# Performance work log

Hardware: AMD Instinct MI355X
Metric: run time of the kernel (lower is better)

The kernel has to match this reference:

```python
import jax, jax.numpy as jnp
import numpy as np

# dims: batch, samples, agents, obs_dim, action_dim, hidden
B, S, N, D, A, H = 512, 64, 8, 64, 16, 256
IN_DIM = (D + A) * N  # 640


def mish(x):
    return x * jnp.tanh(jax.nn.softplus(x))


def setup_inputs() -> dict:
    key = jax.random.key(0)
    ks = jax.random.split(key, 9)
    u = lambda k, shape, fan_in: jax.random.uniform(
        k, shape, jnp.float32, -1.0 / np.sqrt(fan_in), 1.0 / np.sqrt(fan_in))
    return {
        "state": jax.random.normal(ks[0], (B, N, D), jnp.float32),
        "action": jax.random.normal(ks[1], (B, N, A), jnp.float32),
        "W1": u(ks[2], (IN_DIM, H), IN_DIM),
        "b1": u(ks[3], (H,), IN_DIM),
        "W2": u(ks[4], (H, H), H),
        "b2": u(ks[5], (H,), H),
        "W3": u(ks[6], (H, 1), H),
        "b3": u(ks[7], (1,), H),
        # random grand-coalition permutations of the N agents, per (batch, sample)
        "perm": jnp.argsort(jax.random.uniform(ks[8], (B, S, N)), axis=-1).astype(jnp.int32),
    }


def reference(state, action, W1, b1, W2, b2, W3, b3, perm):
    # subcoalition mask [B,S,N,N]: torch builds one-hot(perm) @ tril(ones),
    # i.e. mask[b,s,i,j] = 1 iff j <= perm[b,s,i]
    subcoal = (jnp.arange(N) <= perm[..., None]).astype(state.dtype)
    # gathered actions in coalition order [B,S,N,A]: act_g[b,s,j] = action[b, perm[b,s,j]]
    act_g = action[jnp.arange(B)[:, None, None], perm]
    # masked subcoalition actions [B,S,N,N,A] -> [B,S,N,N*A]
    act = (act_g[:, :, None, :, :] * subcoal[..., None]).reshape(B, S, N, N * A)
    # flattened global obs broadcast over (sample, agent) axes [B,S,N,N*D]
    obs = jnp.broadcast_to(state.reshape(B, 1, 1, N * D), (B, S, N, N * D))
    x = jnp.concatenate([obs, act], axis=-1)  # [B,S,N,IN_DIM]
    # per-agent loop in torch uses shared q1 weights -> single batched MLP
    h = mish(x @ W1 + b1)
    h = mish(h @ W2 + b2)
    q = h @ W3 + b3                   # [B,S,N,1]
    q1 = q.mean(axis=1).squeeze(-1)   # mean over samples -> [B,N]
    return (q1, q1)
```

## Files before the change

### kernel.cpp

```cpp
#include <hip/hip_runtime.h>

typedef unsigned short ushort_t;
typedef _Float16 half_t;
typedef __attribute__((ext_vector_type(2))) _Float16 half2_t;
typedef __attribute__((ext_vector_type(8))) _Float16 half8_t;
typedef __attribute__((ext_vector_type(2))) __fp16 fp16x2;
typedef __attribute__((ext_vector_type(2))) float fx2;
typedef __attribute__((ext_vector_type(4))) float floatx4;

#define LOG2E 1.4426950408889634f
#define LN2   0.6931471805599453f

__device__ __forceinline__ float exp2_(float x) {
#if __has_builtin(__builtin_amdgcn_exp2f)
    return __builtin_amdgcn_exp2f(x);
#else
    return exp2f(x);
#endif
}

__device__ __forceinline__ half2_t cvt_pk_f16(float a, float b) {
    auto r = __builtin_amdgcn_cvt_pkrtz(a, b);
    return __builtin_bit_cast(half2_t, r);
}

__device__ __forceinline__ float fdot2_(half2_t a, half2_t b) {
#if __has_builtin(__builtin_amdgcn_fdot2)
    return __builtin_amdgcn_fdot2(__builtin_bit_cast(fp16x2, a),
                                  __builtin_bit_cast(fp16x2, b), 0.0f, false);
#else
    return (float)a.x * (float)b.x + (float)a.y * (float)b.y;
#endif
}

__device__ __forceinline__ fx2 mish2(fx2 t0) {
    fx2 one = {1.0f, 1.0f};
    fx2 m2  = {-2.0f, -2.0f};
    fx2 u   = {exp2_(t0.x), exp2_(t0.y)};
    fx2 s   = u + one;
    fx2 wv  = __builtin_elementwise_fma(s, s, one);
    fx2 rr  = {__builtin_amdgcn_rcpf(wv.x), __builtin_amdgcn_rcpf(wv.y)};
    fx2 v   = __builtin_elementwise_fma(rr, m2, one);
    return t0 * v;
}

__device__ __forceinline__ float dpp_sum16(float v) {
    int x = __float_as_int(v);
    v += __int_as_float(__builtin_amdgcn_update_dpp(0, x, 0xB1, 0xF, 0xF, true));
    x = __float_as_int(v);
    v += __int_as_float(__builtin_amdgcn_update_dpp(0, x, 0x4E, 0xF, 0xF, true));
    x = __float_as_int(v);
    v += __int_as_float(__builtin_amdgcn_update_dpp(0, x, 0x124, 0xF, 0xF, true));
    x = __float_as_int(v);
    v += __int_as_float(__builtin_amdgcn_update_dpp(0, x, 0x128, 0xF, 0xF, true));
    return v;
}

__global__ __launch_bounds__(256) void prep_kernel(
        const float* __restrict__ state,
        const float* __restrict__ action,
        const float* __restrict__ W1,
        const float* __restrict__ b1,
        const float* __restrict__ W2,
        float* __restrict__ obsW,
        half_t* __restrict__ actW,
        half_t* __restrict__ W2T,
        float* __restrict__ out) {
    int bid = blockIdx.x;
    int t = threadIdx.x;
    if (bid < 512) {
        int b = bid;
        const float* stp = state + (size_t)b * 512;
        const float* w1p = W1 + t;
        float a0 = 0.f, a1 = 0.f, a2 = 0.f, a3 = 0.f;
#pragma unroll 8
        for (int f = 0; f < 512; f += 4) {
            a0 = fmaf(stp[f + 0], w1p[(f + 0) * 256], a0);
            a1 = fmaf(stp[f + 1], w1p[(f + 1) * 256], a1);
            a2 = fmaf(stp[f + 2], w1p[(f + 2) * 256], a2);
            a3 = fmaf(stp[f + 3], w1p[(f + 3) * 256], a3);
        }
        obsW[b * 256 + t] = ((a0 + a1) + (a2 + a3) + b1[t]) * LOG2E;
    } else if (bid < 2560) {
        int idx = bid - 512;
        int j = idx & 7;
        int b0 = (idx >> 3) * 2;
        const float* W1a = W1 + (size_t)(512 + j * 16) * 256;
        float wv[16];
#pragma unroll
        for (int a = 0; a < 16; ++a) wv[a] = W1a[a * 256 + t];
#pragma unroll
        for (int bb = 0; bb < 2; ++bb) {
            int b = b0 + bb;
            const float* acp = action + (size_t)b * 128;
            float acc[8];
#pragma unroll
            for (int n = 0; n < 8; ++n) acc[n] = 0.f;
#pragma unroll
            for (int a = 0; a < 16; ++a) {
#pragma unroll
                for (int n = 0; n < 8; ++n)
                    acc[n] = fmaf(acp[n * 16 + a], wv[a], acc[n]);
            }
#pragma unroll
            for (int n = 0; n < 8; ++n)
                actW[(((size_t)b * 8 + n) * 8 + j) * 256 + t] = (half_t)(acc[n] * LOG2E);
        }
    } else {
        int blk = bid - 2560;
        if (blk < 16) {
            out[blk * 512 + t] = 0.0f;
            out[blk * 512 + 256 + t] = 0.0f;
        }
        int n = blk * 8 + (t >> 5);
        int klo = t & 31;
#pragma unroll
        for (int kk = 0; kk < 8; ++kk) {
            int k = kk * 32 + klo;
            W2T[n * 256 + k] = (half_t)W2[k * 256 + n];
        }
    }
}

#define CHUNK_US 528

__global__ __launch_bounds__(512, 4) void main_kernel(
        const float* __restrict__ obsW, const half_t* __restrict__ actW,
        const half_t* __restrict__ W2T, const int* __restrict__ perm,
        const float* __restrict__ b2,
        const float* __restrict__ W3, const float* __restrict__ b3,
        float* __restrict__ out) {
    __shared__ __align__(16) ushort_t h1[2][32 * CHUNK_US];
    __shared__ __align__(16) float obsb[256];
    __shared__ int perm_s[128];
    __shared__ float qpart[2][8][64];

    int t = threadIdx.x;
    int bid = blockIdx.x;
    int b = (bid & 7) * 64 + ((bid >> 3) & 63);
    int sgp = bid >> 9;
    int s0 = sgp * 16;

    int w = t >> 6;
    int L = t & 63;
    int lo = L & 15;
    int q = L >> 4;

    if (t < 256) obsb[t] = obsW[b * 256 + t];
    else if (t < 384) perm_s[t - 256] = perm[((size_t)b * 64 + s0) * 8 + (t - 256)];

    const half_t* w2base = W2T + ((size_t)(w * 32 + lo)) * 256 + q * 8;
    half8_t bpre[4];
    bpre[0] = *reinterpret_cast<const half8_t*>(w2base + 0 * 4096 + 0 * 32);
    bpre[1] = *reinterpret_cast<const half8_t*>(w2base + 1 * 4096 + 0 * 32);
    bpre[2] = *reinterpret_cast<const half8_t*>(w2base + 0 * 4096 + 1 * 32);
    bpre[3] = *reinterpret_cast<const half8_t*>(w2base + 1 * 4096 + 1 * 32);

    int g = L >> 1;
    int ksg = g >> 2;
    int qq = g & 3;
    int halfsel = L & 1;
    const half_t* actg = actW + (size_t)b * 64 * 256 + L * 4;
    int dstoff = qq * 128 + halfsel * 4 + ksg * CHUNK_US;

    __syncthreads();

    float4 ob = *reinterpret_cast<const float4*>(obsb + L * 4);

    {
        uint2 av[8];
#pragma unroll
        for (int j = 0; j < 8; ++j) {
            int p = perm_s[(0 * 8 + w) * 8 + j];
            av[j] = *reinterpret_cast<const uint2*>(actg + (p * 8 + j) * 256);
        }
        fx2 r01 = {ob.x, ob.y};
        fx2 r23 = {ob.z, ob.w};
        ushort_t* dst0 = h1[0] + dstoff;
#pragma unroll
        for (int j = 0; j < 8; ++j) {
            half2_t a0 = __builtin_bit_cast(half2_t, av[j].x);
            half2_t a1 = __builtin_bit_cast(half2_t, av[j].y);
            r01 += (fx2){(float)a0.x, (float)a0.y};
            r23 += (fx2){(float)a1.x, (float)a1.y};
            fx2 h01 = mish2(r01);
            fx2 h23 = mish2(r23);
            int row = w * 8 + j;
            int mt2 = row >> 4, lr = row & 15;
            uint2 pk = make_uint2(__builtin_bit_cast(unsigned, cvt_pk_f16(h01.x, h01.y)),
                                  __builtin_bit_cast(unsigned, cvt_pk_f16(h23.x, h23.y)));
            *reinterpret_cast<uint2*>(dst0 + mt2 * 8 * CHUNK_US + lr * 8) = pk;
        }
    }
    __syncthreads();

    floatx4 acc0[4][2];
#pragma unroll
    for (int mt = 0; mt < 4; ++mt)
#pragma unroll
        for (int nt = 0; nt < 2; ++nt) acc0[mt][nt] = (floatx4){0.f, 0.f, 0.f, 0.f};
    {
        uint2 av[8];
#pragma unroll
        for (int j = 0; j < 8; ++j) {
            int p = perm_s[(1 * 8 + w) * 8 + j];
            av[j] = *reinterpret_cast<const uint2*>(actg + (p * 8 + j) * 256);
        }
        fx2 r01 = {ob.x, ob.y};
        fx2 r23 = {ob.z, ob.w};
        ushort_t* dst1 = h1[1] + dstoff;
        const ushort_t* h1b0 = h1[0] + L * 8;
#pragma unroll
        for (int ks = 0; ks < 8; ++ks) {
            half8_t afr[4];
#pragma unroll
            for (int mt = 0; mt < 4; ++mt)
                afr[mt] = *reinterpret_cast<const half8_t*>(h1b0 + (mt * 8 + ks) * CHUNK_US);
            half8_t bfr0 = (ks == 0) ? bpre[0] : (ks == 1) ? bpre[2]
                         : *reinterpret_cast<const half8_t*>(w2base + 0 * 4096 + ks * 32);
            half8_t bfr1 = (ks == 0) ? bpre[1] : (ks == 1) ? bpre[3]
                         : *reinterpret_cast<const half8_t*>(w2base + 1 * 4096 + ks * 32);
#pragma unroll
            for (int mt = 0; mt < 4; ++mt) {
                acc0[mt][0] = __builtin_amdgcn_mfma_f32_16x16x32_f16(afr[mt], bfr0, acc0[mt][0], 0, 0, 0);
                acc0[mt][1] = __builtin_amdgcn_mfma_f32_16x16x32_f16(afr[mt], bfr1, acc0[mt][1], 0, 0, 0);
            }
            {
                half2_t a0 = __builtin_bit_cast(half2_t, av[ks].x);
                half2_t a1 = __builtin_bit_cast(half2_t, av[ks].y);
                r01 += (fx2){(float)a0.x, (float)a0.y};
                r23 += (fx2){(float)a1.x, (float)a1.y};
                fx2 h01 = mish2(r01);
                fx2 h23 = mish2(r23);
                int row = w * 8 + ks;
                int mt2 = row >> 4, lr = row & 15;
                uint2 pk = make_uint2(__builtin_bit_cast(unsigned, cvt_pk_f16(h01.x, h01.y)),
                                      __builtin_bit_cast(unsigned, cvt_pk_f16(h23.x, h23.y)));
                *reinterpret_cast<uint2*>(dst1 + mt2 * 8 * CHUNK_US + lr * 8) = pk;
            }
        }
    }
    __syncthreads();

    int col0 = w * 32 + 0 * 16 + lo;
    int col1 = w * 32 + 1 * 16 + lo;
    fx2 b2p = {b2[col0] * LOG2E, b2[col1] * LOG2E};
    half2_t w3p = cvt_pk_f16(W3[col0] * LN2, W3[col1] * LN2);

    floatx4 acc1[4][2];
#pragma unroll
    for (int mt = 0; mt < 4; ++mt)
#pragma unroll
        for (int nt = 0; nt < 2; ++nt) acc1[mt][nt] = (floatx4){0.f, 0.f, 0.f, 0.f};
    {
        const ushort_t* h1b1 = h1[1] + L * 8;
#pragma unroll
        for (int ks = 0; ks < 8; ++ks) {
            half8_t afr[4];
#pragma unroll
            for (int mt = 0; mt < 4; ++mt)
                afr[mt] = *reinterpret_cast<const half8_t*>(h1b1 + (mt * 8 + ks) * CHUNK_US);
            half8_t bfr0 = (ks == 0) ? bpre[0] : (ks == 1) ? bpre[2]
                         : *reinterpret_cast<const half8_t*>(w2base + 0 * 4096 + ks * 32);
            half8_t bfr1 = (ks == 0) ? bpre[1] : (ks == 1) ? bpre[3]
                         : *reinterpret_cast<const half8_t*>(w2base + 1 * 4096 + ks * 32);
#pragma unroll
            for (int mt = 0; mt < 4; ++mt) {
                acc1[mt][0] = __builtin_amdgcn_mfma_f32_16x16x32_f16(afr[mt], bfr0, acc1[mt][0], 0, 0, 0);
                acc1[mt][1] = __builtin_amdgcn_mfma_f32_16x16x32_f16(afr[mt], bfr1, acc1[mt][1], 0, 0, 0);
            }
#pragma unroll
            for (int v = 0; v < 2; ++v) {
                int idx = ks * 2 + v;
                int mt = idx >> 2, r = idx & 3;
                fx2 t2 = {acc0[mt][0][r], acc0[mt][1][r]};
                t2 += b2p;
                fx2 hh = mish2(t2);
                float part = fdot2_(cvt_pk_f16(hh.x, hh.y), w3p);
                float s = dpp_sum16(part);
                if (lo == 0) qpart[0][w][mt * 16 + q * 4 + r] = s;
            }
        }
    }
#pragma unroll
    for (int idx = 0; idx < 16; ++idx) {
        int mt = idx >> 2, r = idx & 3;
        fx2 t2 = {acc1[mt][0][r], acc1[mt][1][r]};
        t2 += b2p;
        fx2 hh = mish2(t2);
        float part = fdot2_(cvt_pk_f16(hh.x, hh.y), w3p);
        float s = dpp_sum16(part);
        if (lo == 0) qpart[1][w][mt * 16 + q * 4 + r] = s;
    }
    __syncthreads();

    if (t < 16) {
        int h = t >> 3, i = t & 7;
        float p = 0.f;
#pragma unroll
        for (int sl = 0; sl < 8; ++sl) {
            int k = perm_s[(h * 8 + sl) * 8 + i];
            int row = sl * 8 + k;
            float qv = b3[0];
#pragma unroll
            for (int ww = 0; ww < 8; ++ww) qv += qpart[h][ww][row];
            p += qv;
        }
        p *= (1.0f / 64.0f);
        atomicAdd(&out[b * 8 + i], p);
        atomicAdd(&out[4096 + b * 8 + i], p);
    }
}

extern "C" void kernel_launch(void* const* d_in, const int* in_sizes, int n_in,
                              void* d_out, int out_size, void* d_ws, size_t ws_size,
                              hipStream_t stream) {
    const float* state  = (const float*)d_in[0];
    const float* action = (const float*)d_in[1];
    const float* W1     = (const float*)d_in[2];
    const float* b1     = (const float*)d_in[3];
    const float* W2     = (const float*)d_in[4];
    const float* b2     = (const float*)d_in[5];
    const float* W3     = (const float*)d_in[6];
    const float* b3     = (const float*)d_in[7];
    const int*   perm   = (const int*)d_in[8];
    float* out = (float*)d_out;

    char* ws = (char*)d_ws;
    float*  obsW = (float*)ws;
    half_t* actW = (half_t*)(ws + 524288);
    half_t* W2T  = (half_t*)(ws + 524288 + 16777216);

    prep_kernel<<<2592, 256, 0, stream>>>(state, action, W1, b1, W2, obsW, actW, W2T, out);
    main_kernel<<<2048, 512, 0, stream>>>(obsW, actW, W2T, perm, b2, W3, b3, out);
}
```

Measured before the change: 165.3 us.

## Process four sample groups per block with a double-buffered software pipeline

Each block now handles 32 samples (four groups of 8) instead of 16, and the grid is halved. A loop over groups overlaps the layer-1 build of the next group and the layer-2 epilogue of the previous group with the MFMA work of the current group. This spreads the per-block setup (obs load, bias and W3 loads, atomics) over more work and lengthens the pipeline. The cost is fewer blocks for latency hiding and a larger live register set for the two accumulator sets. The W2 prefetch registers are dropped.

```diff
diff --git a/kernel.cpp b/kernel.cpp
--- a/kernel.cpp
+++ b/kernel.cpp
@@ -132,14 +132,13 @@
         float* __restrict__ out) {
     __shared__ __align__(16) ushort_t h1[2][32 * CHUNK_US];
     __shared__ __align__(16) float obsb[256];
-    __shared__ int perm_s[128];
-    __shared__ float qpart[2][8][64];
+    __shared__ int perm_s[256];
+    __shared__ float qpart[4][8][64];
 
     int t = threadIdx.x;
     int bid = blockIdx.x;
     int b = (bid & 7) * 64 + ((bid >> 3) & 63);
-    int sgp = bid >> 9;
-    int s0 = sgp * 16;
+    int s0 = (bid >> 9) * 32;
 
     int w = t >> 6;
     int L = t & 63;
@@ -147,22 +146,22 @@
     int q = L >> 4;
 
     if (t < 256) obsb[t] = obsW[b * 256 + t];
-    else if (t < 384) perm_s[t - 256] = perm[((size_t)b * 64 + s0) * 8 + (t - 256)];
+    else perm_s[t - 256] = perm[((size_t)b * 64 + s0) * 8 + (t - 256)];
 
     const half_t* w2base = W2T + ((size_t)(w * 32 + lo)) * 256 + q * 8;
-    half8_t bpre[4];
-    bpre[0] = *reinterpret_cast<const half8_t*>(w2base + 0 * 4096 + 0 * 32);
-    bpre[1] = *reinterpret_cast<const half8_t*>(w2base + 1 * 4096 + 0 * 32);
-    bpre[2] = *reinterpret_cast<const half8_t*>(w2base + 0 * 4096 + 1 * 32);
-    bpre[3] = *reinterpret_cast<const half8_t*>(w2base + 1 * 4096 + 1 * 32);
-
-    int g = L >> 1;
-    int ksg = g >> 2;
-    int qq = g & 3;
+
+    int g2 = L >> 1;
+    int ksg = g2 >> 2;
+    int qq = g2 & 3;
     int halfsel = L & 1;
     const half_t* actg = actW + (size_t)b * 64 * 256 + L * 4;
     int dstoff = qq * 128 + halfsel * 4 + ksg * CHUNK_US;
 
+    int col0 = w * 32 + 0 * 16 + lo;
+    int col1 = w * 32 + 1 * 16 + lo;
+    fx2 b2p = {b2[col0] * LOG2E, b2[col1] * LOG2E};
+    half2_t w3p = cvt_pk_f16(W3[col0] * LN2, W3[col1] * LN2);
+
     __syncthreads();
 
     float4 ob = *reinterpret_cast<const float4*>(obsb + L * 4);
@@ -171,12 +170,12 @@
         uint2 av[8];
 #pragma unroll
         for (int j = 0; j < 8; ++j) {
-            int p = perm_s[(0 * 8 + w) * 8 + j];
+            int p = perm_s[w * 8 + j];
             av[j] = *reinterpret_cast<const uint2*>(actg + (p * 8 + j) * 256);
         }
         fx2 r01 = {ob.x, ob.y};
         fx2 r23 = {ob.z, ob.w};
-        ushort_t* dst0 = h1[0] + dstoff;
+        ushort_t* dst = h1[0] + dstoff;
 #pragma unroll
         for (int j = 0; j < 8; ++j) {
             half2_t a0 = __builtin_bit_cast(half2_t, av[j].x);
@@ -189,43 +188,51 @@
             int mt2 = row >> 4, lr = row & 15;
             uint2 pk = make_uint2(__builtin_bit_cast(unsigned, cvt_pk_f16(h01.x, h01.y)),
                                   __builtin_bit_cast(unsigned, cvt_pk_f16(h23.x, h23.y)));
-            *reinterpret_cast<uint2*>(dst0 + mt2 * 8 * CHUNK_US + lr * 8) = pk;
+            *reinterpret_cast<uint2*>(dst + mt2 * 8 * CHUNK_US + lr * 8) = pk;
         }
     }
     __syncthreads();
 
-    floatx4 acc0[4][2];
-#pragma unroll
-    for (int mt = 0; mt < 4; ++mt)
-#pragma unroll
-        for (int nt = 0; nt < 2; ++nt) acc0[mt][nt] = (floatx4){0.f, 0.f, 0.f, 0.f};
-    {
+    floatx4 acc[2][4][2];
+
+#pragma unroll
+    for (int g = 0; g < 4; ++g) {
+        int cur = g & 1;
+        int nxt = cur ^ 1;
+#pragma unroll
+        for (int mt = 0; mt < 4; ++mt)
+#pragma unroll
+            for (int nt = 0; nt < 2; ++nt)
+                acc[cur][mt][nt] = (floatx4){0.f, 0.f, 0.f, 0.f};
+
         uint2 av[8];
-#pragma unroll
-        for (int j = 0; j < 8; ++j) {
-            int p = perm_s[(1 * 8 + w) * 8 + j];
-            av[j] = *reinterpret_cast<const uint2*>(actg + (p * 8 + j) * 256);
-        }
-        fx2 r01 = {ob.x, ob.y};
-        fx2 r23 = {ob.z, ob.w};
-        ushort_t* dst1 = h1[1] + dstoff;
-        const ushort_t* h1b0 = h1[0] + L * 8;
+        fx2 r01, r23;
+        if (g < 3) {
+#pragma unroll
+            for (int j = 0; j < 8; ++j) {
+                int p = perm_s[(g + 1) * 64 + w * 8 + j];
+                av[j] = *reinterpret_cast<const uint2*>(actg + (p * 8 + j) * 256);
+            }
+            r01 = (fx2){ob.x, ob.y};
+            r23 = (fx2){ob.z, ob.w};
+        }
+        const ushort_t* h1b = h1[cur] + L * 8;
+        ushort_t* dst = h1[nxt] + dstoff;
+
 #pragma unroll
         for (int ks = 0; ks < 8; ++ks) {
             half8_t afr[4];
 #pragma unroll
             for (int mt = 0; mt < 4; ++mt)
-                afr[mt] = *reinterpret_cast<const half8_t*>(h1b0 + (mt * 8 + ks) * CHUNK_US);
-            half8_t bfr0 = (ks == 0) ? bpre[0] : (ks == 1) ? bpre[2]
-                         : *reinterpret_cast<const half8_t*>(w2base + 0 * 4096 + ks * 32);
-            half8_t bfr1 = (ks == 0) ? bpre[1] : (ks == 1) ? bpre[3]
-                         : *reinterpret_cast<const half8_t*>(w2base + 1 * 4096 + ks * 32);
+                afr[mt] = *reinterpret_cast<const half8_t*>(h1b + (mt * 8 + ks) * CHUNK_US);
+            half8_t bfr0 = *reinterpret_cast<const half8_t*>(w2base + 0 * 4096 + ks * 32);
+            half8_t bfr1 = *reinterpret_cast<const half8_t*>(w2base + 1 * 4096 + ks * 32);
 #pragma unroll
             for (int mt = 0; mt < 4; ++mt) {
-                acc0[mt][0] = __builtin_amdgcn_mfma_f32_16x16x32_f16(afr[mt], bfr0, acc0[mt][0], 0, 0, 0);
-                acc0[mt][1] = __builtin_amdgcn_mfma_f32_16x16x32_f16(afr[mt], bfr1, acc0[mt][1], 0, 0, 0);
-            }
-            {
+                acc[cur][mt][0] = __builtin_amdgcn_mfma_f32_16x16x32_f16(afr[mt], bfr0, acc[cur][mt][0], 0, 0, 0);
+                acc[cur][mt][1] = __builtin_amdgcn_mfma_f32_16x16x32_f16(afr[mt], bfr1, acc[cur][mt][1], 0, 0, 0);
+            }
+            if (g < 3) {
                 half2_t a0 = __builtin_bit_cast(half2_t, av[ks].x);
                 half2_t a1 = __builtin_bit_cast(half2_t, av[ks].y);
                 r01 += (fx2){(float)a0.x, (float)a0.y};
@@ -236,65 +243,39 @@
                 int mt2 = row >> 4, lr = row & 15;
                 uint2 pk = make_uint2(__builtin_bit_cast(unsigned, cvt_pk_f16(h01.x, h01.y)),
                                       __builtin_bit_cast(unsigned, cvt_pk_f16(h23.x, h23.y)));
-                *reinterpret_cast<uint2*>(dst1 + mt2 * 8 * CHUNK_US + lr * 8) = pk;
-            }
-        }
-    }
-    __syncthreads();
-
-    int col0 = w * 32 + 0 * 16 + lo;
-    int col1 = w * 32 + 1 * 16 + lo;
-    fx2 b2p = {b2[col0] * LOG2E, b2[col1] * LOG2E};
-    half2_t w3p = cvt_pk_f16(W3[col0] * LN2, W3[col1] * LN2);
-
-    floatx4 acc1[4][2];
-#pragma unroll
-    for (int mt = 0; mt < 4; ++mt)
-#pragma unroll
-        for (int nt = 0; nt < 2; ++nt) acc1[mt][nt] = (floatx4){0.f, 0.f, 0.f, 0.f};
-    {
-        const ushort_t* h1b1 = h1[1] + L * 8;
-#pragma unroll
-        for (int ks = 0; ks < 8; ++ks) {
-            half8_t afr[4];
-#pragma unroll
-            for (int mt = 0; mt < 4; ++mt)
-                afr[mt] = *reinterpret_cast<const half8_t*>(h1b1 + (mt * 8 + ks) * CHUNK_US);
-            half8_t bfr0 = (ks == 0) ? bpre[0] : (ks == 1) ? bpre[2]
-                         : *reinterpret_cast<const half8_t*>(w2base + 0 * 4096 + ks * 32);
-            half8_t bfr1 = (ks == 0) ? bpre[1] : (ks == 1) ? bpre[3]
-                         : *reinterpret_cast<const half8_t*>(w2base + 1 * 4096 + ks * 32);
-#pragma unroll
-            for (int mt = 0; mt < 4; ++mt) {
-                acc1[mt][0] = __builtin_amdgcn_mfma_f32_16x16x32_f16(afr[mt], bfr0, acc1[mt][0], 0, 0, 0);
-                acc1[mt][1] = __builtin_amdgcn_mfma_f32_16x16x32_f16(afr[mt], bfr1, acc1[mt][1], 0, 0, 0);
-            }
-#pragma unroll
-            for (int v = 0; v < 2; ++v) {
-                int idx = ks * 2 + v;
-                int mt = idx >> 2, r = idx & 3;
-                fx2 t2 = {acc0[mt][0][r], acc0[mt][1][r]};
-                t2 += b2p;
-                fx2 hh = mish2(t2);
-                float part = fdot2_(cvt_pk_f16(hh.x, hh.y), w3p);
-                float s = dpp_sum16(part);
-                if (lo == 0) qpart[0][w][mt * 16 + q * 4 + r] = s;
-            }
-        }
-    }
+                *reinterpret_cast<uint2*>(dst + mt2 * 8 * CHUNK_US + lr * 8) = pk;
+            }
+            if (g > 0) {
+                int prv = cur ^ 1;
+#pragma unroll
+                for (int v = 0; v < 2; ++v) {
+                    int idx = ks * 2 + v;
+                    int mt = idx >> 2, r = idx & 3;
+                    fx2 t2 = {acc[prv][mt][0][r], acc[prv][mt][1][r]};
+                    t2 += b2p;
+                    fx2 hh = mish2(t2);
+                    float part = fdot2_(cvt_pk_f16(hh.x, hh.y), w3p);
+                    float s = dpp_sum16(part);
+                    if (lo == 0) qpart[g - 1][w][mt * 16 + q * 4 + r] = s;
+                }
+            }
+        }
+        __syncthreads();
+    }
+
 #pragma unroll
     for (int idx = 0; idx < 16; ++idx) {
         int mt = idx >> 2, r = idx & 3;
-        fx2 t2 = {acc1[mt][0][r], acc1[mt][1][r]};
+        fx2 t2 = {acc[1][mt][0][r], acc[1][mt][1][r]};
         t2 += b2p;
         fx2 hh = mish2(t2);
         float part = fdot2_(cvt_pk_f16(hh.x, hh.y), w3p);
         float s = dpp_sum16(part);
-        if (lo == 0) qpart[1][w][mt * 16 + q * 4 + r] = s;
+        if (lo == 0) qpart[3][w][mt * 16 + q * 4 + r] = s;
     }
     __syncthreads();
 
-    if (t < 16) {
+    if (t < 32) {
         int h = t >> 3, i = t & 7;
         float p = 0.f;
 #pragma unroll
@@ -332,5 +313,5 @@
     half_t* W2T  = (half_t*)(ws + 524288 + 16777216);
 
     prep_kernel<<<2592, 256, 0, stream>>>(state, action, W1, b1, W2, obsW, actW, W2T, out);
-    main_kernel<<<2048, 512, 0, stream>>>(obsW, actW, W2T, perm, b2, W3, b3, out);
-}
+    main_kernel<<<1024, 512, 0, stream>>>(obsW, actW, W2T, perm, b2, W3, b3, out);
+}
```

New measurement: 173.3 us. 4.8% more time.

## Split obs projection over K chunks with batch reuse; reduce partials in main kernel

Applied to the files above, without the earlier changes.

The obs-times-W1 projection in the prep kernel is reorganised so each block handles 8 batches and one 64-wide K chunk. Each W1 load is reused across 8 batch rows instead of 1, and the block count is unchanged. The 8 partial sums go to a larger workspace and are reduced, with bias and LOG2E scaling, when the main kernel loads obsb. The action projection also doubles its batches per block to reuse loaded weights, which cuts the prep grid. In exchange the main kernel does 8 extra global loads per thread and the workspace grows.

```diff
diff --git a/kernel.cpp b/kernel.cpp
--- a/kernel.cpp
+++ b/kernel.cpp
@@ -60,37 +60,42 @@
         const float* __restrict__ state,
         const float* __restrict__ action,
         const float* __restrict__ W1,
-        const float* __restrict__ b1,
         const float* __restrict__ W2,
-        float* __restrict__ obsW,
+        float* __restrict__ obsWp,
         half_t* __restrict__ actW,
         half_t* __restrict__ W2T,
         float* __restrict__ out) {
     int bid = blockIdx.x;
     int t = threadIdx.x;
     if (bid < 512) {
-        int b = bid;
-        const float* stp = state + (size_t)b * 512;
-        const float* w1p = W1 + t;
-        float a0 = 0.f, a1 = 0.f, a2 = 0.f, a3 = 0.f;
-#pragma unroll 8
-        for (int f = 0; f < 512; f += 4) {
-            a0 = fmaf(stp[f + 0], w1p[(f + 0) * 256], a0);
-            a1 = fmaf(stp[f + 1], w1p[(f + 1) * 256], a1);
-            a2 = fmaf(stp[f + 2], w1p[(f + 2) * 256], a2);
-            a3 = fmaf(stp[f + 3], w1p[(f + 3) * 256], a3);
-        }
-        obsW[b * 256 + t] = ((a0 + a1) + (a2 + a3) + b1[t]) * LOG2E;
-    } else if (bid < 2560) {
+        int bg = bid >> 3;
+        int kc = bid & 7;
+        int bs = bg * 8;
+        const float* w1p = W1 + (size_t)(kc * 64) * 256 + t;
+        const float* stp = state + (size_t)bs * 512 + kc * 64;
+        float acc[8];
+#pragma unroll
+        for (int bb = 0; bb < 8; ++bb) acc[bb] = 0.f;
+#pragma unroll 4
+        for (int f = 0; f < 64; ++f) {
+            float w = w1p[f * 256];
+#pragma unroll
+            for (int bb = 0; bb < 8; ++bb)
+                acc[bb] = fmaf(stp[bb * 512 + f], w, acc[bb]);
+        }
+#pragma unroll
+        for (int bb = 0; bb < 8; ++bb)
+            obsWp[(size_t)kc * 131072 + (bs + bb) * 256 + t] = acc[bb];
+    } else if (bid < 1536) {
         int idx = bid - 512;
         int j = idx & 7;
-        int b0 = (idx >> 3) * 2;
+        int b0 = (idx >> 3) * 4;
         const float* W1a = W1 + (size_t)(512 + j * 16) * 256;
         float wv[16];
 #pragma unroll
         for (int a = 0; a < 16; ++a) wv[a] = W1a[a * 256 + t];
 #pragma unroll
-        for (int bb = 0; bb < 2; ++bb) {
+        for (int bb = 0; bb < 4; ++bb) {
             int b = b0 + bb;
             const float* acp = action + (size_t)b * 128;
             float acc[8];
@@ -107,7 +112,7 @@
                 actW[(((size_t)b * 8 + n) * 8 + j) * 256 + t] = (half_t)(acc[n] * LOG2E);
         }
     } else {
-        int blk = bid - 2560;
+        int blk = bid - 1536;
         if (blk < 16) {
             out[blk * 512 + t] = 0.0f;
             out[blk * 512 + 256 + t] = 0.0f;
@@ -125,9 +130,9 @@
 #define CHUNK_US 528
 
 __global__ __launch_bounds__(512, 4) void main_kernel(
-        const float* __restrict__ obsW, const half_t* __restrict__ actW,
+        const float* __restrict__ obsWp, const half_t* __restrict__ actW,
         const half_t* __restrict__ W2T, const int* __restrict__ perm,
-        const float* __restrict__ b2,
+        const float* __restrict__ b1, const float* __restrict__ b2,
         const float* __restrict__ W3, const float* __restrict__ b3,
         float* __restrict__ out) {
     __shared__ __align__(16) ushort_t h1[2][32 * CHUNK_US];
@@ -146,8 +151,14 @@
     int lo = L & 15;
     int q = L >> 4;
 
-    if (t < 256) obsb[t] = obsW[b * 256 + t];
-    else if (t < 384) perm_s[t - 256] = perm[((size_t)b * 64 + s0) * 8 + (t - 256)];
+    if (t < 256) {
+        float s = b1[t];
+#pragma unroll
+        for (int c = 0; c < 8; ++c) s += obsWp[(size_t)c * 131072 + b * 256 + t];
+        obsb[t] = s * LOG2E;
+    } else if (t < 384) {
+        perm_s[t - 256] = perm[((size_t)b * 64 + s0) * 8 + (t - 256)];
+    }
 
     const half_t* w2base = W2T + ((size_t)(w * 32 + lo)) * 256 + q * 8;
     half8_t bpre[4];
@@ -327,10 +338,10 @@
     float* out = (float*)d_out;
 
     char* ws = (char*)d_ws;
-    float*  obsW = (float*)ws;
-    half_t* actW = (half_t*)(ws + 524288);
-    half_t* W2T  = (half_t*)(ws + 524288 + 16777216);
-
-    prep_kernel<<<2592, 256, 0, stream>>>(state, action, W1, b1, W2, obsW, actW, W2T, out);
-    main_kernel<<<2048, 512, 0, stream>>>(obsW, actW, W2T, perm, b2, W3, b3, out);
-}
+    float*  obsWp = (float*)ws;
+    half_t* actW  = (half_t*)(ws + 4194304);
+    half_t* W2T   = (half_t*)(ws + 4194304 + 16777216);
+
+    prep_kernel<<<1568, 256, 0, stream>>>(state, action, W1, W2, obsWp, actW, W2T, out);
+    main_kernel<<<2048, 512, 0, stream>>>(obsWp, actW, W2T, perm, b1, b2, W3, b3, out);
+}
```

New measurement: 163.7 us, median of 2. Within noise of the previous version (-0.9%).
